# Kernel optimization log

Measured on AMD Instinct MI355X. Metric: run time of the kernel, lower is better.

## Reference

```python
import jax, jax.numpy as jnp
import numpy as np

B_, T_, M_, R_, S_ = 2, 2048, 768, 64, 16
LOG_EPS = float(np.log(1e-10))

def setup_inputs() -> dict:
    key = jax.random.key(0)
    ks = jax.random.split(key, 8)
    u = jax.random.normal(ks[0], (B_, T_, M_), jnp.float32)
    delta = jax.random.normal(ks[1], (B_, T_, R_), jnp.float32)
    # dt_proj weights kept small and bias strongly negative so softplus(dt) is
    # small -> cumulative log-decay over T=2048 stays in a numerically safe range
    dt_w = jax.random.normal(ks[2], (M_, R_), jnp.float32) * 1e-3
    dt_b = -8.0 + 0.1 * jax.random.normal(ks[3], (M_,), jnp.float32)
    # A_log ~ Uniform(-3, -1) as in nn.init.uniform_(self.A_log, -3.0, -1.0)
    A_log = jax.random.uniform(ks[4], (S_, M_), jnp.float32, minval=-3.0, maxval=-1.0)
    # xavier_uniform with gain=0.1 ~ small weights
    B_w = jax.random.normal(ks[5], (S_, M_), jnp.float32) * 0.005
    C_w = jax.random.normal(ks[6], (S_, M_), jnp.float32) * 0.005
    D = jnp.ones((M_,), jnp.float32)
    return dict(u=u, delta=delta, dt_w=dt_w, dt_b=dt_b, A_log=A_log, B_w=B_w, C_w=C_w, D=D)

def reference(u, delta, dt_w, dt_b, A_log, B_w, C_w, D):
    # delta = clamp(softplus(dt_proj(delta)))            [b,t,m]
    dt = jax.nn.softplus(jnp.einsum('btr,mr->btm', delta, dt_w) + dt_b)
    dt = jnp.clip(dt, 1e-6, 10.0)
    # A = clamp(-exp(A_log))                             [s,m]
    A = jnp.clip(-jnp.exp(A_log), -10.0, -1e-6)
    Bm = jnp.einsum('btm,sm->bts', u, B_w)               # B_proj(u)
    Cm = jnp.einsum('btm,sm->bts', u, C_w)               # C_proj(u)
    # discretization: deltaA = dt * A, deltaB_u = dt * B * u   [b,t,s,m]
    dA = dt[:, :, None, :] * A                           # log of exp(dt*A)
    dBu = dt[:, :, None, :] * Bm[..., None] * u[:, :, None, :]
    # associative scan via cumsum in log space (module's clamp(1e-10) -> floor log)
    cum_log_A = jnp.cumsum(jnp.maximum(dA, LOG_EPS), axis=1)   # [b,t,s,m]
    A_cum = jnp.exp(cum_log_A)
    # h_t = (prod_{k<=t} a_k) * sum_{k<=t} x_k / (prod_{j<=k} a_j)
    h = A_cum * jnp.cumsum(dBu * jnp.exp(-cum_log_A), axis=1)  # [b,t,s,m]
    y = jnp.einsum('btsm,bts->btm', h, Cm)
    out = jnp.clip(y + u * D, -1e4, 1e4)
    # module's NaN/Inf fallback to zeros, expressed jit-compatibly
    bad = jnp.any(~jnp.isfinite(out))
    return jnp.where(bad, jnp.zeros_like(out), out)
```

## Files before the change

kernel.cpp:

```cpp
#include <hip/hip_runtime.h>
#include <math.h>

#define B_ 2
#define T_ 2048
#define M_ 768
#define R_ 64
#define S_ 16
#define MS_ (M_ * S_)
#define NC 128
#define CL (T_ / NC)
#define LOG_EPS_F (-23.025850929940457f)

__global__ __launch_bounds__(256) void dt_kernel(
    const float* __restrict__ delta,
    const float* __restrict__ dt_w,
    const float* __restrict__ dt_b,
    float* __restrict__ dt_out)
{
  __shared__ float ds_d[R_][68];
  __shared__ float ds_w[R_][68];
  const int tid = threadIdx.x;
  const int m0  = blockIdx.x * 64;
  const int bt0 = blockIdx.y * 64;

  #pragma unroll
  for (int k = 0; k < 4; ++k) {
    int idx = tid + k * 256;
    int rq = idx & 15;
    int x  = idx >> 4;
    float4 dv = *reinterpret_cast<const float4*>(&delta[(size_t)(bt0 + x) * R_ + rq * 4]);
    ds_d[rq * 4 + 0][x] = dv.x; ds_d[rq * 4 + 1][x] = dv.y;
    ds_d[rq * 4 + 2][x] = dv.z; ds_d[rq * 4 + 3][x] = dv.w;
    float4 wv = *reinterpret_cast<const float4*>(&dt_w[(size_t)(m0 + x) * R_ + rq * 4]);
    ds_w[rq * 4 + 0][x] = wv.x; ds_w[rq * 4 + 1][x] = wv.y;
    ds_w[rq * 4 + 2][x] = wv.z; ds_w[rq * 4 + 3][x] = wv.w;
  }
  __syncthreads();

  const int mq = tid & 15, tq = tid >> 4;
  const int ml = mq * 4, tl = tq * 4;
  float acc[4][4] = {};
  #pragma unroll 4
  for (int r = 0; r < R_; ++r) {
    float4 dv = *reinterpret_cast<const float4*>(&ds_d[r][tl]);
    float4 wv = *reinterpret_cast<const float4*>(&ds_w[r][ml]);
    float d[4] = {dv.x, dv.y, dv.z, dv.w};
    float w[4] = {wv.x, wv.y, wv.z, wv.w};
    #pragma unroll
    for (int i = 0; i < 4; ++i)
      #pragma unroll
      for (int j = 0; j < 4; ++j)
        acc[i][j] = fmaf(d[i], w[j], acc[i][j]);
  }

  float4 bb = *reinterpret_cast<const float4*>(&dt_b[m0 + ml]);
  float bv[4] = {bb.x, bb.y, bb.z, bb.w};
  #pragma unroll
  for (int i = 0; i < 4; ++i) {
    float4 o;
    float* op = &o.x;
    #pragma unroll
    for (int j = 0; j < 4; ++j) {
      float x = acc[i][j] + bv[j];
      float sp = (x > 20.f) ? x : __logf(1.f + __expf(x));
      op[j] = fminf(fmaxf(sp, 1e-6f), 10.f);
    }
    *reinterpret_cast<float4*>(&dt_out[(size_t)(bt0 + tl + i) * M_ + m0 + ml]) = o;
  }
}

__global__ __launch_bounds__(512, 4) void bc_kernel(
    const float* __restrict__ u,
    const float* __restrict__ B_w,
    const float* __restrict__ C_w,
    float* __restrict__ Bm,
    float* __restrict__ Cm)
{
  const int wave = threadIdx.x >> 6, lane = threadIdx.x & 63;
  const int bt0 = blockIdx.x * 8;

  float4 w[4][3];
  #pragma unroll
  for (int s = 0; s < 4; ++s) {
    const int s_g = wave * 4 + s;
    const float* wr = (s_g < 16) ? &B_w[(size_t)s_g * M_] : &C_w[(size_t)(s_g - 16) * M_];
    const float4* w4 = reinterpret_cast<const float4*>(wr);
    w[s][0] = w4[lane]; w[s][1] = w4[64 + lane]; w[s][2] = w4[128 + lane];
  }

  float acc[32];
  #pragma unroll
  for (int r = 0; r < 8; ++r) {
    const float4* ur = reinterpret_cast<const float4*>(&u[(size_t)(bt0 + r) * M_]);
    const float4 a0 = ur[lane], a1 = ur[64 + lane], a2 = ur[128 + lane];
    #pragma unroll
    for (int s = 0; s < 4; ++s) {
      float t = 0.f;
      t = fmaf(a0.x, w[s][0].x, t); t = fmaf(a0.y, w[s][0].y, t);
      t = fmaf(a0.z, w[s][0].z, t); t = fmaf(a0.w, w[s][0].w, t);
      t = fmaf(a1.x, w[s][1].x, t); t = fmaf(a1.y, w[s][1].y, t);
      t = fmaf(a1.z, w[s][1].z, t); t = fmaf(a1.w, w[s][1].w, t);
      t = fmaf(a2.x, w[s][2].x, t); t = fmaf(a2.y, w[s][2].y, t);
      t = fmaf(a2.z, w[s][2].z, t); t = fmaf(a2.w, w[s][2].w, t);
      acc[r * 4 + s] = t;
    }
  }

  #pragma unroll
  for (int j = 0; j < 32; ++j) acc[j] += __shfl_xor(acc[j], 32);
  int cnt = 32;
  #pragma unroll
  for (int mask = 16; mask >= 1; mask >>= 1) {
    cnt >>= 1;
    const bool up = (lane & mask) != 0;
    #pragma unroll
    for (int j = 0; j < cnt; ++j) {
      float give = up ? acc[j] : acc[j + cnt];
      float keep = up ? acc[j + cnt] : acc[j];
      acc[j] = keep + __shfl_xor(give, mask);
    }
  }

  if (lane < 32) {
    const int r = lane >> 2, s_l = lane & 3;
    const int s_g = wave * 4 + s_l;
    const int bt = bt0 + r;
    if (s_g < 16) Bm[(size_t)bt * S_ + s_g] = acc[0];
    else          Cm[(size_t)bt * S_ + (s_g - 16)] = acc[0];
  }
}

template <int PHASE>
__global__ __launch_bounds__(128) void scan_kernel(
    const float* __restrict__ dt_ws,
    const float* __restrict__ u,
    const float* __restrict__ Bm,
    const float* __restrict__ Cm,
    const float* __restrict__ A_log,
    const float* __restrict__ D,
    float* __restrict__ Aprod,
    float* __restrict__ Hend,
    float* __restrict__ out)
{
  __shared__ float dt_lds[CL][64];
  __shared__ float u_lds[CL][64];
  __shared__ float lds_bm[CL * S_];
  __shared__ float lds_cm[CL * S_];

  const int tid = threadIdx.x;
  const int lane = tid & 63, wv = tid >> 6;
  const int m_l = wv * 32 + (lane & 31);
  const int sh = lane >> 5, s0 = sh * 8;
  const int m = blockIdx.x * 64 + m_l;
  const int c = blockIdx.y, b = blockIdx.z;
  const int t0 = c * CL;

  const size_t gbase = ((size_t)b * T_ + t0) * M_ + blockIdx.x * 64;
  #pragma unroll
  for (int p = 0; p < CL * 16 / 128; ++p) {
    const int i4 = tid + p * 128;
    const int t = i4 >> 4, m4 = (i4 & 15) * 4;
    *reinterpret_cast<float4*>(&dt_lds[t][m4]) =
        *reinterpret_cast<const float4*>(&dt_ws[gbase + (size_t)t * M_ + m4]);
    *reinterpret_cast<float4*>(&u_lds[t][m4]) =
        *reinterpret_cast<const float4*>(&u[gbase + (size_t)t * M_ + m4]);
  }
  {
    const size_t bcb = ((size_t)b * T_ + t0) * S_;
    #pragma unroll
    for (int p = 0; p < CL * S_ / 128; ++p) {
      const int idx = tid + p * 128;
      lds_bm[idx] = Bm[bcb + idx];
      if constexpr (PHASE == 3) lds_cm[idx] = Cm[bcb + idx];
    }
  }

  float Acol[8];
  #pragma unroll
  for (int s = 0; s < 8; ++s) {
    float a = -__expf(A_log[(size_t)(s0 + s) * M_ + m]);
    Acol[s] = fminf(fmaxf(a, -10.f), -1e-6f);
  }

  float h[8], P[8], Dm = 0.f;
  const size_t smb = (((size_t)b * NC + c) * S_ + s0) * M_ + m;
  if constexpr (PHASE == 1) {
    #pragma unroll
    for (int s = 0; s < 8; ++s) { h[s] = 0.f; P[s] = 1.f; }
  } else {
    #pragma unroll
    for (int s = 0; s < 8; ++s) h[s] = Aprod[smb + (size_t)s * M_];
    Dm = D[m];
  }

  __syncthreads();

  const size_t g0 = ((size_t)b * T_ + t0) * M_ + m;
  #pragma unroll 8
  for (int t = 0; t < CL; ++t) {
    const float dtv = dt_lds[t][m_l];
    const float uv  = u_lds[t][m_l];
    const float du  = dtv * uv;
    const float4 bv0 = *reinterpret_cast<const float4*>(&lds_bm[t * S_ + s0]);
    const float4 bv1 = *reinterpret_cast<const float4*>(&lds_bm[t * S_ + s0 + 4]);
    const float bmv[8] = {bv0.x, bv0.y, bv0.z, bv0.w, bv1.x, bv1.y, bv1.z, bv1.w};
    float cmv[8];
    if constexpr (PHASE == 3) {
      const float4 cv0 = *reinterpret_cast<const float4*>(&lds_cm[t * S_ + s0]);
      const float4 cv1 = *reinterpret_cast<const float4*>(&lds_cm[t * S_ + s0 + 4]);
      cmv[0] = cv0.x; cmv[1] = cv0.y; cmv[2] = cv0.z; cmv[3] = cv0.w;
      cmv[4] = cv1.x; cmv[5] = cv1.y; cmv[6] = cv1.z; cmv[7] = cv1.w;
    }
    float y = 0.f;
    #pragma unroll
    for (int s = 0; s < 8; ++s) {
      float la = fmaxf(dtv * Acol[s], LOG_EPS_F);
      float e = __expf(la);
      h[s] = fmaf(e, h[s], du * bmv[s]);
      if constexpr (PHASE == 1) P[s] *= e;
      else y = fmaf(h[s], cmv[s], y);
    }
    if constexpr (PHASE == 3) {
      y += __shfl_xor(y, 32);
      if (sh == 0) {
        float o = y + uv * Dm;
        out[g0 + (size_t)t * M_] = fminf(fmaxf(o, -1e4f), 1e4f);
      }
    }
  }

  if constexpr (PHASE == 1) {
    #pragma unroll
    for (int s = 0; s < 8; ++s) {
      Aprod[smb + (size_t)s * M_] = P[s];
      Hend[smb + (size_t)s * M_]  = h[s];
    }
  }
}

__global__ __launch_bounds__(256) void carry_kernel(
    float* __restrict__ Aprod, const float* __restrict__ Hend)
{
  const int idx = blockIdx.x * 256 + threadIdx.x;
  const int b = idx / MS_;
  const int sm = idx - b * MS_;
  float h = 0.f;
  #pragma unroll 16
  for (int c = 0; c < NC; ++c) {
    const size_t o = ((size_t)b * NC + c) * MS_ + sm;
    const float a  = Aprod[o];
    const float he = Hend[o];
    Aprod[o] = h;
    h = fmaf(a, h, he);
  }
}

extern "C" void kernel_launch(void* const* d_in, const int* in_sizes, int n_in,
                              void* d_out, int out_size, void* d_ws, size_t ws_size,
                              hipStream_t stream)
{
  const float* u     = (const float*)d_in[0];
  const float* delta = (const float*)d_in[1];
  const float* dt_w  = (const float*)d_in[2];
  const float* dt_b  = (const float*)d_in[3];
  const float* A_log = (const float*)d_in[4];
  const float* B_w   = (const float*)d_in[5];
  const float* C_w   = (const float*)d_in[6];
  const float* D     = (const float*)d_in[7];
  float* out = (float*)d_out;
  float* ws  = (float*)d_ws;

  const size_t fl_dt = (size_t)B_ * T_ * M_;
  const size_t fl_bc = (size_t)B_ * T_ * S_;
  const size_t fl_sm = (size_t)B_ * NC * MS_;

  float* dt_ws = ws;
  float* Bm    = dt_ws + fl_dt;
  float* Cm    = Bm + fl_bc;
  float* Aprod = Cm + fl_bc;
  float* Hend  = Aprod + fl_sm;

  dt_kernel<<<dim3(M_ / 64, (B_ * T_) / 64), 256, 0, stream>>>(delta, dt_w, dt_b, dt_ws);
  bc_kernel<<<dim3((B_ * T_) / 8), 512, 0, stream>>>(u, B_w, C_w, Bm, Cm);
  scan_kernel<1><<<dim3(M_ / 64, NC, B_), 128, 0, stream>>>(
      dt_ws, u, Bm, Cm, A_log, D, Aprod, Hend, nullptr);
  carry_kernel<<<dim3((B_ * MS_) / 256), 256, 0, stream>>>(Aprod, Hend);
  scan_kernel<3><<<dim3(M_ / 64, NC, B_), 128, 0, stream>>>(
      dt_ws, u, Bm, Cm, A_log, D, Aprod, Hend, out);
}
```

Before: 70.32 us.

## Process four chunks per scan block with register double-buffered prefetch

Each scan block now handles four consecutive chunks instead of one, loading dt and u straight into registers and prefetching the next chunk's data (including B/C into a second LDS buffer and carried state) while the current chunk is scanned. The decay now uses exp2 with A pre-scaled by log2(e), and phase 1 accumulates the log-sum and applies one exp2 at the end instead of multiplying per step. The aim is to hide global-load latency and reduce per-block setup, at the cost of a quarter as many blocks (fewer waves in flight) and higher register pressure from the 64 prefetch registers.

```diff
diff --git a/kernel.cpp b/kernel.cpp
--- a/kernel.cpp
+++ b/kernel.cpp
@@ -8,8 +8,11 @@
 #define S_ 16
 #define MS_ (M_ * S_)
 #define NC 128
-#define CL (T_ / NC)
-#define LOG_EPS_F (-23.025850929940457f)
+#define CL 16
+#define NCPB 4
+#define NCG (NC / NCPB)
+#define LOG2E 1.4426950408889634f
+#define LOG2_EPS (-33.219280948873623f)
 
 __global__ __launch_bounds__(256) void dt_kernel(
     const float* __restrict__ delta,
@@ -130,8 +133,78 @@
   }
 }
 
+#define PREFETCH_CHUNK(cc, DT, U, HP, NB0, NB1, NCV0, NCV1)                    \
+  {                                                                            \
+    const size_t prow = (size_t)b * T_ + (size_t)(cc) * CL;                    \
+    _Pragma("unroll")                                                          \
+    for (int k = 0; k < CL; ++k) {                                             \
+      DT[k] = dt_ws[(prow + k) * M_ + m];                                      \
+      U[k]  = u[(prow + k) * M_ + m];                                          \
+    }                                                                          \
+    NB0 = Bm[prow * S_ + tid];                                                 \
+    NB1 = Bm[prow * S_ + tid + 128];                                           \
+    if constexpr (PHASE == 3) {                                                \
+      NCV0 = Cm[prow * S_ + tid];                                              \
+      NCV1 = Cm[prow * S_ + tid + 128];                                        \
+      const size_t psmb = (((size_t)b * NC + (cc)) * S_ + s0) * M_ + m;        \
+      _Pragma("unroll")                                                        \
+      for (int s = 0; s < 8; ++s) HP[s] = Aprod[psmb + (size_t)s * M_];        \
+    }                                                                          \
+  }
+
+#define SCAN_CHUNK(cc, DT, U, BUF, HP)                                         \
+  {                                                                            \
+    const size_t srow = (size_t)b * T_ + (size_t)(cc) * CL;                    \
+    float h[8], Sl[8];                                                         \
+    if constexpr (PHASE == 1) {                                                \
+      _Pragma("unroll")                                                        \
+      for (int s = 0; s < 8; ++s) { h[s] = 0.f; Sl[s] = 0.f; }                 \
+    } else {                                                                   \
+      _Pragma("unroll")                                                        \
+      for (int s = 0; s < 8; ++s) h[s] = HP[s];                                \
+    }                                                                          \
+    _Pragma("unroll")                                                          \
+    for (int t = 0; t < CL; ++t) {                                             \
+      const float du = DT[t] * U[t];                                           \
+      const float4 bv0 = *reinterpret_cast<const float4*>(&bm_lds[BUF][t * S_ + s0]);      \
+      const float4 bv1 = *reinterpret_cast<const float4*>(&bm_lds[BUF][t * S_ + s0 + 4]);  \
+      const float bmv[8] = {bv0.x, bv0.y, bv0.z, bv0.w, bv1.x, bv1.y, bv1.z, bv1.w};       \
+      float cmv[8];                                                            \
+      if constexpr (PHASE == 3) {                                              \
+        const float4 cv0 = *reinterpret_cast<const float4*>(&cm_lds[BUF][t * S_ + s0]);     \
+        const float4 cv1 = *reinterpret_cast<const float4*>(&cm_lds[BUF][t * S_ + s0 + 4]); \
+        cmv[0] = cv0.x; cmv[1] = cv0.y; cmv[2] = cv0.z; cmv[3] = cv0.w;        \
+        cmv[4] = cv1.x; cmv[5] = cv1.y; cmv[6] = cv1.z; cmv[7] = cv1.w;        \
+      }                                                                        \
+      float y = 0.f;                                                           \
+      _Pragma("unroll")                                                        \
+      for (int s = 0; s < 8; ++s) {                                            \
+        const float la = fmaxf(DT[t] * A2[s], LOG2_EPS);                       \
+        const float e = exp2f(la);                                             \
+        h[s] = fmaf(e, h[s], du * bmv[s]);                                     \
+        if constexpr (PHASE == 1) Sl[s] += la;                                 \
+        else y = fmaf(h[s], cmv[s], y);                                        \
+      }                                                                        \
+      if constexpr (PHASE == 3) {                                              \
+        y += __shfl_xor(y, 32);                                                \
+        if (sh == 0) {                                                         \
+          const float o = y + U[t] * Dm;                                       \
+          out[(srow + t) * M_ + m] = fminf(fmaxf(o, -1e4f), 1e4f);             \
+        }                                                                      \
+      }                                                                        \
+    }                                                                          \
+    if constexpr (PHASE == 1) {                                                \
+      const size_t wsmb = (((size_t)b * NC + (cc)) * S_ + s0) * M_ + m;        \
+      _Pragma("unroll")                                                        \
+      for (int s = 0; s < 8; ++s) {                                            \
+        Aprod[wsmb + (size_t)s * M_] = exp2f(Sl[s]);                           \
+        Hend[wsmb + (size_t)s * M_]  = h[s];                                   \
+      }                                                                        \
+    }                                                                          \
+  }
+
 template <int PHASE>
-__global__ __launch_bounds__(128) void scan_kernel(
+__global__ __launch_bounds__(128) void scan_v7(
     const float* __restrict__ dt_ws,
     const float* __restrict__ u,
     const float* __restrict__ Bm,
@@ -142,98 +215,72 @@
     float* __restrict__ Hend,
     float* __restrict__ out)
 {
-  __shared__ float dt_lds[CL][64];
-  __shared__ float u_lds[CL][64];
-  __shared__ float lds_bm[CL * S_];
-  __shared__ float lds_cm[CL * S_];
+  __shared__ float bm_lds[2][CL * S_];
+  __shared__ float cm_lds[2][CL * S_];
 
   const int tid = threadIdx.x;
+  const int mt = blockIdx.x;
+  const int cg = blockIdx.y;
+  const int b  = blockIdx.z;
+  const int m0 = mt * 64;
+  const int c0 = cg * NCPB;
+
   const int lane = tid & 63, wv = tid >> 6;
   const int m_l = wv * 32 + (lane & 31);
   const int sh = lane >> 5, s0 = sh * 8;
-  const int m = blockIdx.x * 64 + m_l;
-  const int c = blockIdx.y, b = blockIdx.z;
-  const int t0 = c * CL;
-
-  const size_t gbase = ((size_t)b * T_ + t0) * M_ + blockIdx.x * 64;
-  #pragma unroll
-  for (int p = 0; p < CL * 16 / 128; ++p) {
-    const int i4 = tid + p * 128;
-    const int t = i4 >> 4, m4 = (i4 & 15) * 4;
-    *reinterpret_cast<float4*>(&dt_lds[t][m4]) =
-        *reinterpret_cast<const float4*>(&dt_ws[gbase + (size_t)t * M_ + m4]);
-    *reinterpret_cast<float4*>(&u_lds[t][m4]) =
-        *reinterpret_cast<const float4*>(&u[gbase + (size_t)t * M_ + m4]);
-  }
+  const int m = m0 + m_l;
+
+  float A2[8];
+  #pragma unroll
+  for (int s = 0; s < 8; ++s) {
+    const float a = -__expf(A_log[(size_t)(s0 + s) * M_ + m]);
+    A2[s] = fminf(fmaxf(a, -10.f), -1e-6f) * LOG2E;
+  }
+  float Dm = 0.f;
+  if constexpr (PHASE == 3) Dm = D[m];
+
+  float dtA[CL], uA[CL], dtB[CL], uB[CL];
+  float hpA[8], hpB[8];
+  float nb0, nb1, ncv0, ncv1;
+  (void)hpA; (void)hpB; (void)ncv0; (void)ncv1;
+
   {
-    const size_t bcb = ((size_t)b * T_ + t0) * S_;
-    #pragma unroll
-    for (int p = 0; p < CL * S_ / 128; ++p) {
-      const int idx = tid + p * 128;
-      lds_bm[idx] = Bm[bcb + idx];
-      if constexpr (PHASE == 3) lds_cm[idx] = Cm[bcb + idx];
-    }
-  }
-
-  float Acol[8];
-  #pragma unroll
-  for (int s = 0; s < 8; ++s) {
-    float a = -__expf(A_log[(size_t)(s0 + s) * M_ + m]);
-    Acol[s] = fminf(fmaxf(a, -10.f), -1e-6f);
-  }
-
-  float h[8], P[8], Dm = 0.f;
-  const size_t smb = (((size_t)b * NC + c) * S_ + s0) * M_ + m;
-  if constexpr (PHASE == 1) {
-    #pragma unroll
-    for (int s = 0; s < 8; ++s) { h[s] = 0.f; P[s] = 1.f; }
-  } else {
-    #pragma unroll
-    for (int s = 0; s < 8; ++s) h[s] = Aprod[smb + (size_t)s * M_];
-    Dm = D[m];
-  }
-
+    const size_t prow = (size_t)b * T_ + (size_t)c0 * CL;
+    #pragma unroll
+    for (int k = 0; k < CL; ++k) {
+      dtA[k] = dt_ws[(prow + k) * M_ + m];
+      uA[k]  = u[(prow + k) * M_ + m];
+    }
+    bm_lds[0][tid]       = Bm[prow * S_ + tid];
+    bm_lds[0][tid + 128] = Bm[prow * S_ + tid + 128];
+    if constexpr (PHASE == 3) {
+      cm_lds[0][tid]       = Cm[prow * S_ + tid];
+      cm_lds[0][tid + 128] = Cm[prow * S_ + tid + 128];
+      const size_t psmb = (((size_t)b * NC + c0) * S_ + s0) * M_ + m;
+      #pragma unroll
+      for (int s = 0; s < 8; ++s) hpA[s] = Aprod[psmb + (size_t)s * M_];
+    }
+  }
   __syncthreads();
 
-  const size_t g0 = ((size_t)b * T_ + t0) * M_ + m;
-  #pragma unroll 8
-  for (int t = 0; t < CL; ++t) {
-    const float dtv = dt_lds[t][m_l];
-    const float uv  = u_lds[t][m_l];
-    const float du  = dtv * uv;
-    const float4 bv0 = *reinterpret_cast<const float4*>(&lds_bm[t * S_ + s0]);
-    const float4 bv1 = *reinterpret_cast<const float4*>(&lds_bm[t * S_ + s0 + 4]);
-    const float bmv[8] = {bv0.x, bv0.y, bv0.z, bv0.w, bv1.x, bv1.y, bv1.z, bv1.w};
-    float cmv[8];
-    if constexpr (PHASE == 3) {
-      const float4 cv0 = *reinterpret_cast<const float4*>(&lds_cm[t * S_ + s0]);
-      const float4 cv1 = *reinterpret_cast<const float4*>(&lds_cm[t * S_ + s0 + 4]);
-      cmv[0] = cv0.x; cmv[1] = cv0.y; cmv[2] = cv0.z; cmv[3] = cv0.w;
-      cmv[4] = cv1.x; cmv[5] = cv1.y; cmv[6] = cv1.z; cmv[7] = cv1.w;
-    }
-    float y = 0.f;
-    #pragma unroll
-    for (int s = 0; s < 8; ++s) {
-      float la = fmaxf(dtv * Acol[s], LOG_EPS_F);
-      float e = __expf(la);
-      h[s] = fmaf(e, h[s], du * bmv[s]);
-      if constexpr (PHASE == 1) P[s] *= e;
-      else y = fmaf(h[s], cmv[s], y);
-    }
-    if constexpr (PHASE == 3) {
-      y += __shfl_xor(y, 32);
-      if (sh == 0) {
-        float o = y + uv * Dm;
-        out[g0 + (size_t)t * M_] = fminf(fmaxf(o, -1e4f), 1e4f);
-      }
-    }
-  }
-
-  if constexpr (PHASE == 1) {
-    #pragma unroll
-    for (int s = 0; s < 8; ++s) {
-      Aprod[smb + (size_t)s * M_] = P[s];
-      Hend[smb + (size_t)s * M_]  = h[s];
+  #pragma unroll
+  for (int cp = 0; cp < NCPB / 2; ++cp) {
+    const int cA = c0 + cp * 2;
+
+    PREFETCH_CHUNK(cA + 1, dtB, uB, hpB, nb0, nb1, ncv0, ncv1);
+    SCAN_CHUNK(cA, dtA, uA, 0, hpA);
+    bm_lds[1][tid] = nb0; bm_lds[1][tid + 128] = nb1;
+    if constexpr (PHASE == 3) { cm_lds[1][tid] = ncv0; cm_lds[1][tid + 128] = ncv1; }
+    __syncthreads();
+
+    if (cp < NCPB / 2 - 1) {
+      PREFETCH_CHUNK(cA + 2, dtA, uA, hpA, nb0, nb1, ncv0, ncv1);
+    }
+    SCAN_CHUNK(cA + 1, dtB, uB, 1, hpB);
+    if (cp < NCPB / 2 - 1) {
+      bm_lds[0][tid] = nb0; bm_lds[0][tid + 128] = nb1;
+      if constexpr (PHASE == 3) { cm_lds[0][tid] = ncv0; cm_lds[0][tid + 128] = ncv1; }
+      __syncthreads();
     }
   }
 }
@@ -282,9 +329,9 @@
 
   dt_kernel<<<dim3(M_ / 64, (B_ * T_) / 64), 256, 0, stream>>>(delta, dt_w, dt_b, dt_ws);
   bc_kernel<<<dim3((B_ * T_) / 8), 512, 0, stream>>>(u, B_w, C_w, Bm, Cm);
-  scan_kernel<1><<<dim3(M_ / 64, NC, B_), 128, 0, stream>>>(
+  scan_v7<1><<<dim3(M_ / 64, NCG, B_), 128, 0, stream>>>(
       dt_ws, u, Bm, Cm, A_log, D, Aprod, Hend, nullptr);
   carry_kernel<<<dim3((B_ * MS_) / 256), 256, 0, stream>>>(Aprod, Hend);
-  scan_kernel<3><<<dim3(M_ / 64, NC, B_), 128, 0, stream>>>(
+  scan_v7<3><<<dim3(M_ / 64, NCG, B_), 128, 0, stream>>>(
       dt_ws, u, Bm, Cm, A_log, D, Aprod, Hend, out);
 }
```

Result: slower. 93.14 us (+32.4%).

## Merge dt and B/C projections into one launch; batch exp2 work in scan

Applied to the files above, without the earlier changes.

The separate dt projection and B/C projection kernels become one launch. Block index selects which branch a block runs, and dt tiles grow to 128 rows by 512 threads, saving a launch and letting both projections overlap. The scan kernel now works in base 2 with exp2f and a pre-scaled A. It computes the decay factors for groups of four timesteps before the dependent recurrence, exposing more instruction-level parallelism. Phase 1 accumulates the sum of log-decays and does a single exp2 at the end instead of a running product, which slightly changes rounding.

```diff
diff --git a/kernel.cpp b/kernel.cpp
--- a/kernel.cpp
+++ b/kernel.cpp
@@ -8,130 +8,140 @@
 #define S_ 16
 #define MS_ (M_ * S_)
 #define NC 128
-#define CL (T_ / NC)
-#define LOG_EPS_F (-23.025850929940457f)
-
-__global__ __launch_bounds__(256) void dt_kernel(
+#define CL 16
+#define LOG2E 1.4426950408889634f
+#define LOG2_EPS (-33.219280948873623f)
+
+__global__ __launch_bounds__(512, 4) void proj_kernel(
+    const float* __restrict__ u,
     const float* __restrict__ delta,
     const float* __restrict__ dt_w,
     const float* __restrict__ dt_b,
-    float* __restrict__ dt_out)
-{
-  __shared__ float ds_d[R_][68];
-  __shared__ float ds_w[R_][68];
-  const int tid = threadIdx.x;
-  const int m0  = blockIdx.x * 64;
-  const int bt0 = blockIdx.y * 64;
-
-  #pragma unroll
-  for (int k = 0; k < 4; ++k) {
-    int idx = tid + k * 256;
-    int rq = idx & 15;
-    int x  = idx >> 4;
-    float4 dv = *reinterpret_cast<const float4*>(&delta[(size_t)(bt0 + x) * R_ + rq * 4]);
-    ds_d[rq * 4 + 0][x] = dv.x; ds_d[rq * 4 + 1][x] = dv.y;
-    ds_d[rq * 4 + 2][x] = dv.z; ds_d[rq * 4 + 3][x] = dv.w;
-    float4 wv = *reinterpret_cast<const float4*>(&dt_w[(size_t)(m0 + x) * R_ + rq * 4]);
-    ds_w[rq * 4 + 0][x] = wv.x; ds_w[rq * 4 + 1][x] = wv.y;
-    ds_w[rq * 4 + 2][x] = wv.z; ds_w[rq * 4 + 3][x] = wv.w;
-  }
-  __syncthreads();
-
-  const int mq = tid & 15, tq = tid >> 4;
-  const int ml = mq * 4, tl = tq * 4;
-  float acc[4][4] = {};
-  #pragma unroll 4
-  for (int r = 0; r < R_; ++r) {
-    float4 dv = *reinterpret_cast<const float4*>(&ds_d[r][tl]);
-    float4 wv = *reinterpret_cast<const float4*>(&ds_w[r][ml]);
-    float d[4] = {dv.x, dv.y, dv.z, dv.w};
-    float w[4] = {wv.x, wv.y, wv.z, wv.w};
-    #pragma unroll
-    for (int i = 0; i < 4; ++i)
-      #pragma unroll
-      for (int j = 0; j < 4; ++j)
-        acc[i][j] = fmaf(d[i], w[j], acc[i][j]);
-  }
-
-  float4 bb = *reinterpret_cast<const float4*>(&dt_b[m0 + ml]);
-  float bv[4] = {bb.x, bb.y, bb.z, bb.w};
-  #pragma unroll
-  for (int i = 0; i < 4; ++i) {
-    float4 o;
-    float* op = &o.x;
-    #pragma unroll
-    for (int j = 0; j < 4; ++j) {
-      float x = acc[i][j] + bv[j];
-      float sp = (x > 20.f) ? x : __logf(1.f + __expf(x));
-      op[j] = fminf(fmaxf(sp, 1e-6f), 10.f);
-    }
-    *reinterpret_cast<float4*>(&dt_out[(size_t)(bt0 + tl + i) * M_ + m0 + ml]) = o;
-  }
-}
-
-__global__ __launch_bounds__(512, 4) void bc_kernel(
-    const float* __restrict__ u,
     const float* __restrict__ B_w,
     const float* __restrict__ C_w,
+    float* __restrict__ dt_out,
     float* __restrict__ Bm,
     float* __restrict__ Cm)
 {
-  const int wave = threadIdx.x >> 6, lane = threadIdx.x & 63;
-  const int bt0 = blockIdx.x * 8;
-
-  float4 w[4][3];
-  #pragma unroll
-  for (int s = 0; s < 4; ++s) {
-    const int s_g = wave * 4 + s;
-    const float* wr = (s_g < 16) ? &B_w[(size_t)s_g * M_] : &C_w[(size_t)(s_g - 16) * M_];
-    const float4* w4 = reinterpret_cast<const float4*>(wr);
-    w[s][0] = w4[lane]; w[s][1] = w4[64 + lane]; w[s][2] = w4[128 + lane];
-  }
-
-  float acc[32];
-  #pragma unroll
-  for (int r = 0; r < 8; ++r) {
-    const float4* ur = reinterpret_cast<const float4*>(&u[(size_t)(bt0 + r) * M_]);
-    const float4 a0 = ur[lane], a1 = ur[64 + lane], a2 = ur[128 + lane];
+  __shared__ float ds_d[R_][132];
+  __shared__ float ds_w[R_][68];
+
+  const int tid = threadIdx.x;
+
+  if (blockIdx.x < 512) {
+    const int wave = tid >> 6, lane = tid & 63;
+    const int bt0 = blockIdx.x * 8;
+
+    float4 w[4][3];
     #pragma unroll
     for (int s = 0; s < 4; ++s) {
-      float t = 0.f;
-      t = fmaf(a0.x, w[s][0].x, t); t = fmaf(a0.y, w[s][0].y, t);
-      t = fmaf(a0.z, w[s][0].z, t); t = fmaf(a0.w, w[s][0].w, t);
-      t = fmaf(a1.x, w[s][1].x, t); t = fmaf(a1.y, w[s][1].y, t);
-      t = fmaf(a1.z, w[s][1].z, t); t = fmaf(a1.w, w[s][1].w, t);
-      t = fmaf(a2.x, w[s][2].x, t); t = fmaf(a2.y, w[s][2].y, t);
-      t = fmaf(a2.z, w[s][2].z, t); t = fmaf(a2.w, w[s][2].w, t);
-      acc[r * 4 + s] = t;
-    }
-  }
-
-  #pragma unroll
-  for (int j = 0; j < 32; ++j) acc[j] += __shfl_xor(acc[j], 32);
-  int cnt = 32;
-  #pragma unroll
-  for (int mask = 16; mask >= 1; mask >>= 1) {
-    cnt >>= 1;
-    const bool up = (lane & mask) != 0;
-    #pragma unroll
-    for (int j = 0; j < cnt; ++j) {
-      float give = up ? acc[j] : acc[j + cnt];
-      float keep = up ? acc[j + cnt] : acc[j];
-      acc[j] = keep + __shfl_xor(give, mask);
-    }
-  }
-
-  if (lane < 32) {
-    const int r = lane >> 2, s_l = lane & 3;
-    const int s_g = wave * 4 + s_l;
-    const int bt = bt0 + r;
-    if (s_g < 16) Bm[(size_t)bt * S_ + s_g] = acc[0];
-    else          Cm[(size_t)bt * S_ + (s_g - 16)] = acc[0];
+      const int s_g = wave * 4 + s;
+      const float* wr = (s_g < 16) ? &B_w[(size_t)s_g * M_] : &C_w[(size_t)(s_g - 16) * M_];
+      const float4* w4 = reinterpret_cast<const float4*>(wr);
+      w[s][0] = w4[lane]; w[s][1] = w4[64 + lane]; w[s][2] = w4[128 + lane];
+    }
+
+    float acc[32];
+    #pragma unroll
+    for (int r = 0; r < 8; ++r) {
+      const float4* ur = reinterpret_cast<const float4*>(&u[(size_t)(bt0 + r) * M_]);
+      const float4 a0 = ur[lane], a1 = ur[64 + lane], a2 = ur[128 + lane];
+      #pragma unroll
+      for (int s = 0; s < 4; ++s) {
+        float t = 0.f;
+        t = fmaf(a0.x, w[s][0].x, t); t = fmaf(a0.y, w[s][0].y, t);
+        t = fmaf(a0.z, w[s][0].z, t); t = fmaf(a0.w, w[s][0].w, t);
+        t = fmaf(a1.x, w[s][1].x, t); t = fmaf(a1.y, w[s][1].y, t);
+        t = fmaf(a1.z, w[s][1].z, t); t = fmaf(a1.w, w[s][1].w, t);
+        t = fmaf(a2.x, w[s][2].x, t); t = fmaf(a2.y, w[s][2].y, t);
+        t = fmaf(a2.z, w[s][2].z, t); t = fmaf(a2.w, w[s][2].w, t);
+        acc[r * 4 + s] = t;
+      }
+    }
+
+    #pragma unroll
+    for (int j = 0; j < 32; ++j) acc[j] += __shfl_xor(acc[j], 32);
+    int cnt = 32;
+    #pragma unroll
+    for (int mask = 16; mask >= 1; mask >>= 1) {
+      cnt >>= 1;
+      const bool up = (lane & mask) != 0;
+      #pragma unroll
+      for (int j = 0; j < cnt; ++j) {
+        float give = up ? acc[j] : acc[j + cnt];
+        float keep = up ? acc[j + cnt] : acc[j];
+        acc[j] = keep + __shfl_xor(give, mask);
+      }
+    }
+
+    if (lane < 32) {
+      const int r = lane >> 2, s_l = lane & 3;
+      const int s_g = wave * 4 + s_l;
+      const int bt = bt0 + r;
+      if (s_g < 16) Bm[(size_t)bt * S_ + s_g] = acc[0];
+      else          Cm[(size_t)bt * S_ + (s_g - 16)] = acc[0];
+    }
+  } else {
+    const int bid2 = blockIdx.x - 512;
+    const int mt = bid2 % (M_ / 64);
+    const int bt0 = (bid2 / (M_ / 64)) * 128;
+    const int m0 = mt * 64;
+
+    #pragma unroll
+    for (int k = 0; k < 4; ++k) {
+      int idx = tid + k * 512;
+      int rq = idx & 15;
+      int x  = idx >> 4;
+      float4 dv = *reinterpret_cast<const float4*>(&delta[(size_t)(bt0 + x) * R_ + rq * 4]);
+      ds_d[rq * 4 + 0][x] = dv.x; ds_d[rq * 4 + 1][x] = dv.y;
+      ds_d[rq * 4 + 2][x] = dv.z; ds_d[rq * 4 + 3][x] = dv.w;
+    }
+    #pragma unroll
+    for (int k = 0; k < 2; ++k) {
+      int idx = tid + k * 512;
+      int rq = idx & 15;
+      int x  = idx >> 4;
+      float4 wv = *reinterpret_cast<const float4*>(&dt_w[(size_t)(m0 + x) * R_ + rq * 4]);
+      ds_w[rq * 4 + 0][x] = wv.x; ds_w[rq * 4 + 1][x] = wv.y;
+      ds_w[rq * 4 + 2][x] = wv.z; ds_w[rq * 4 + 3][x] = wv.w;
+    }
+    __syncthreads();
+
+    const int mq = tid & 15, tq = tid >> 4;
+    const int ml = mq * 4, tl = tq * 4;
+    float acc[4][4] = {};
+    #pragma unroll 4
+    for (int r = 0; r < R_; ++r) {
+      float4 dv = *reinterpret_cast<const float4*>(&ds_d[r][tl]);
+      float4 wv = *reinterpret_cast<const float4*>(&ds_w[r][ml]);
+      float d[4] = {dv.x, dv.y, dv.z, dv.w};
+      float w[4] = {wv.x, wv.y, wv.z, wv.w};
+      #pragma unroll
+      for (int i = 0; i < 4; ++i)
+        #pragma unroll
+        for (int j = 0; j < 4; ++j)
+          acc[i][j] = fmaf(d[i], w[j], acc[i][j]);
+    }
+
+    float4 bb = *reinterpret_cast<const float4*>(&dt_b[m0 + ml]);
+    float bv[4] = {bb.x, bb.y, bb.z, bb.w};
+    #pragma unroll
+    for (int i = 0; i < 4; ++i) {
+      float4 o;
+      float* op = &o.x;
+      #pragma unroll
+      for (int j = 0; j < 4; ++j) {
+        float x = acc[i][j] + bv[j];
+        float sp = (x > 20.f) ? x : __logf(1.f + __expf(x));
+        op[j] = fminf(fmaxf(sp, 1e-6f), 10.f);
+      }
+      *reinterpret_cast<float4*>(&dt_out[(size_t)(bt0 + tl + i) * M_ + m0 + ml]) = o;
+    }
   }
 }
 
 template <int PHASE>
-__global__ __launch_bounds__(128) void scan_kernel(
+__global__ __launch_bounds__(128) void scan_v8(
     const float* __restrict__ dt_ws,
     const float* __restrict__ u,
     const float* __restrict__ Bm,
@@ -144,95 +154,106 @@
 {
   __shared__ float dt_lds[CL][64];
   __shared__ float u_lds[CL][64];
-  __shared__ float lds_bm[CL * S_];
-  __shared__ float lds_cm[CL * S_];
+  __shared__ float bm_lds[CL * S_];
+  __shared__ float cm_lds[CL * S_];
 
   const int tid = threadIdx.x;
+  const int mt = blockIdx.x;
+  const int c  = blockIdx.y;
+  const int b  = blockIdx.z;
+  const int m0 = mt * 64;
+  const size_t row0 = (size_t)b * T_ + (size_t)c * CL;
+
+  #pragma unroll
+  for (int p = 0; p < 2; ++p) {
+    const int i4 = tid + p * 128;
+    const int t = i4 >> 4, m4 = (i4 & 15) * 4;
+    *reinterpret_cast<float4*>(&dt_lds[t][m4]) =
+        *reinterpret_cast<const float4*>(&dt_ws[(row0 + t) * M_ + m0 + m4]);
+    *reinterpret_cast<float4*>(&u_lds[t][m4]) =
+        *reinterpret_cast<const float4*>(&u[(row0 + t) * M_ + m0 + m4]);
+  }
+  {
+    const size_t bcb = row0 * S_;
+    bm_lds[tid]       = Bm[bcb + tid];
+    bm_lds[tid + 128] = Bm[bcb + tid + 128];
+    if constexpr (PHASE == 3) {
+      cm_lds[tid]       = Cm[bcb + tid];
+      cm_lds[tid + 128] = Cm[bcb + tid + 128];
+    }
+  }
+
   const int lane = tid & 63, wv = tid >> 6;
   const int m_l = wv * 32 + (lane & 31);
   const int sh = lane >> 5, s0 = sh * 8;
-  const int m = blockIdx.x * 64 + m_l;
-  const int c = blockIdx.y, b = blockIdx.z;
-  const int t0 = c * CL;
-
-  const size_t gbase = ((size_t)b * T_ + t0) * M_ + blockIdx.x * 64;
-  #pragma unroll
-  for (int p = 0; p < CL * 16 / 128; ++p) {
-    const int i4 = tid + p * 128;
-    const int t = i4 >> 4, m4 = (i4 & 15) * 4;
-    *reinterpret_cast<float4*>(&dt_lds[t][m4]) =
-        *reinterpret_cast<const float4*>(&dt_ws[gbase + (size_t)t * M_ + m4]);
-    *reinterpret_cast<float4*>(&u_lds[t][m4]) =
-        *reinterpret_cast<const float4*>(&u[gbase + (size_t)t * M_ + m4]);
-  }
-  {
-    const size_t bcb = ((size_t)b * T_ + t0) * S_;
-    #pragma unroll
-    for (int p = 0; p < CL * S_ / 128; ++p) {
-      const int idx = tid + p * 128;
-      lds_bm[idx] = Bm[bcb + idx];
-      if constexpr (PHASE == 3) lds_cm[idx] = Cm[bcb + idx];
-    }
-  }
-
-  float Acol[8];
+  const int m = m0 + m_l;
+
+  float A2[8];
   #pragma unroll
   for (int s = 0; s < 8; ++s) {
-    float a = -__expf(A_log[(size_t)(s0 + s) * M_ + m]);
-    Acol[s] = fminf(fmaxf(a, -10.f), -1e-6f);
-  }
-
-  float h[8], P[8], Dm = 0.f;
+    const float a = -__expf(A_log[(size_t)(s0 + s) * M_ + m]);
+    A2[s] = fminf(fmaxf(a, -10.f), -1e-6f) * LOG2E;
+  }
+
+  float h[8], Sla[8], Dm = 0.f;
   const size_t smb = (((size_t)b * NC + c) * S_ + s0) * M_ + m;
   if constexpr (PHASE == 1) {
     #pragma unroll
-    for (int s = 0; s < 8; ++s) { h[s] = 0.f; P[s] = 1.f; }
+    for (int s = 0; s < 8; ++s) { h[s] = 0.f; Sla[s] = 0.f; }
   } else {
     #pragma unroll
     for (int s = 0; s < 8; ++s) h[s] = Aprod[smb + (size_t)s * M_];
     Dm = D[m];
   }
-
   __syncthreads();
 
-  const size_t g0 = ((size_t)b * T_ + t0) * M_ + m;
-  #pragma unroll 8
-  for (int t = 0; t < CL; ++t) {
-    const float dtv = dt_lds[t][m_l];
-    const float uv  = u_lds[t][m_l];
-    const float du  = dtv * uv;
-    const float4 bv0 = *reinterpret_cast<const float4*>(&lds_bm[t * S_ + s0]);
-    const float4 bv1 = *reinterpret_cast<const float4*>(&lds_bm[t * S_ + s0 + 4]);
-    const float bmv[8] = {bv0.x, bv0.y, bv0.z, bv0.w, bv1.x, bv1.y, bv1.z, bv1.w};
-    float cmv[8];
-    if constexpr (PHASE == 3) {
-      const float4 cv0 = *reinterpret_cast<const float4*>(&lds_cm[t * S_ + s0]);
-      const float4 cv1 = *reinterpret_cast<const float4*>(&lds_cm[t * S_ + s0 + 4]);
-      cmv[0] = cv0.x; cmv[1] = cv0.y; cmv[2] = cv0.z; cmv[3] = cv0.w;
-      cmv[4] = cv1.x; cmv[5] = cv1.y; cmv[6] = cv1.z; cmv[7] = cv1.w;
-    }
-    float y = 0.f;
+  #pragma unroll
+  for (int tg = 0; tg < CL; tg += 4) {
+    float e[4][8], dus[4];
+    #pragma unroll
+    for (int k = 0; k < 4; ++k) {
+      const float dtv = dt_lds[tg + k][m_l];
+      dus[k] = dtv * u_lds[tg + k][m_l];
+      #pragma unroll
+      for (int s = 0; s < 8; ++s) {
+        const float la = fmaxf(dtv * A2[s], LOG2_EPS);
+        e[k][s] = exp2f(la);
+        if constexpr (PHASE == 1) Sla[s] += la;
+      }
+    }
+    #pragma unroll
+    for (int k = 0; k < 4; ++k) {
+      const int t = tg + k;
+      const float4 bv0 = *reinterpret_cast<const float4*>(&bm_lds[t * S_ + s0]);
+      const float4 bv1 = *reinterpret_cast<const float4*>(&bm_lds[t * S_ + s0 + 4]);
+      const float bmv[8] = {bv0.x, bv0.y, bv0.z, bv0.w, bv1.x, bv1.y, bv1.z, bv1.w};
+      float cmv[8];
+      if constexpr (PHASE == 3) {
+        const float4 cv0 = *reinterpret_cast<const float4*>(&cm_lds[t * S_ + s0]);
+        const float4 cv1 = *reinterpret_cast<const float4*>(&cm_lds[t * S_ + s0 + 4]);
+        cmv[0] = cv0.x; cmv[1] = cv0.y; cmv[2] = cv0.z; cmv[3] = cv0.w;
+        cmv[4] = cv1.x; cmv[5] = cv1.y; cmv[6] = cv1.z; cmv[7] = cv1.w;
+      }
+      float y = 0.f;
+      #pragma unroll
+      for (int s = 0; s < 8; ++s) {
+        h[s] = fmaf(e[k][s], h[s], dus[k] * bmv[s]);
+        if constexpr (PHASE == 3) y = fmaf(h[s], cmv[s], y);
+      }
+      if constexpr (PHASE == 3) {
+        y += __shfl_xor(y, 32);
+        if (sh == 0) {
+          const float o = y + u_lds[t][m_l] * Dm;
+          out[(row0 + t) * M_ + m] = fminf(fmaxf(o, -1e4f), 1e4f);
+        }
+      }
+    }
+  }
+
+  if constexpr (PHASE == 1) {
     #pragma unroll
     for (int s = 0; s < 8; ++s) {
-      float la = fmaxf(dtv * Acol[s], LOG_EPS_F);
-      float e = __expf(la);
-      h[s] = fmaf(e, h[s], du * bmv[s]);
-      if constexpr (PHASE == 1) P[s] *= e;
-      else y = fmaf(h[s], cmv[s], y);
-    }
-    if constexpr (PHASE == 3) {
-      y += __shfl_xor(y, 32);
-      if (sh == 0) {
-        float o = y + uv * Dm;
-        out[g0 + (size_t)t * M_] = fminf(fmaxf(o, -1e4f), 1e4f);
-      }
-    }
-  }
-
-  if constexpr (PHASE == 1) {
-    #pragma unroll
-    for (int s = 0; s < 8; ++s) {
-      Aprod[smb + (size_t)s * M_] = P[s];
+      Aprod[smb + (size_t)s * M_] = exp2f(Sla[s]);
       Hend[smb + (size_t)s * M_]  = h[s];
     }
   }
@@ -280,11 +301,11 @@
   float* Aprod = Cm + fl_bc;
   float* Hend  = Aprod + fl_sm;
 
-  dt_kernel<<<dim3(M_ / 64, (B_ * T_) / 64), 256, 0, stream>>>(delta, dt_w, dt_b, dt_ws);
-  bc_kernel<<<dim3((B_ * T_) / 8), 512, 0, stream>>>(u, B_w, C_w, Bm, Cm);
-  scan_kernel<1><<<dim3(M_ / 64, NC, B_), 128, 0, stream>>>(
+  proj_kernel<<<dim3(512 + (M_ / 64) * ((B_ * T_) / 128)), 512, 0, stream>>>(
+      u, delta, dt_w, dt_b, B_w, C_w, dt_ws, Bm, Cm);
+  scan_v8<1><<<dim3(M_ / 64, NC, B_), 128, 0, stream>>>(
       dt_ws, u, Bm, Cm, A_log, D, Aprod, Hend, nullptr);
   carry_kernel<<<dim3((B_ * MS_) / 256), 256, 0, stream>>>(Aprod, Hend);
-  scan_kernel<3><<<dim3(M_ / 64, NC, B_), 128, 0, stream>>>(
+  scan_v8<3><<<dim3(M_ / 64, NC, B_), 128, 0, stream>>>(
       dt_ws, u, Bm, Cm, A_log, D, Aprod, Hend, out);
 }
```

After: 80.48 us. +14.4%, slower.
